# Kernel tuning notes

Measured on AMD Instinct MI355X. Metric: run time of the kernel, lower is better.

## Reference

```python
import jax, jax.numpy as jnp
import numpy as np
from jax import lax

# Static config (mirrors Caps2dMatwo init_kwargs)
K_SIZE = 5
T1 = 8              # num_capsule (output capsule types)
POS = (4, 4)
APP = (4, 4)
ROUTINGS = 3
COORD_ADD = True
ZP = POS[0] * POS[1]   # 16
ZA = APP[0] * APP[1]   # 16
Z = ZP + ZA            # 32 == input channels z_0


def _psquash(p, axis):
    return p / jnp.max(jnp.abs(p), axis=axis, keepdims=True)


def _matwo_squash(p, axis):
    n2 = jnp.sum(p * p, axis=axis, keepdims=True)
    n = jnp.sqrt(n2 + 1e-9)
    return n2 / (1.0 + n2) * p / n


def _coord_const(H, W):
    # coordinate_addition: adds normalized (x, y) into last row of the pos matrix
    yy, xx = np.meshgrid(np.arange(H), np.arange(W), indexing='ij')
    c = np.zeros((H * W, 1, POS[1], POS[1]), np.float32)
    c[:, 0, -1, 0] = xx.reshape(-1) / W
    c[:, 0, -1, 1] = yy.reshape(-1) / H
    return jnp.asarray(c)


def setup_inputs() -> dict:
    key = jax.random.key(0)
    k1, k2, k3, k4, k5 = jax.random.split(key, 5)
    N, T0, H, W = 4, 4, 96, 96
    return {
        'input_tensor': jax.random.normal(k1, (N, T0, Z, H, W), jnp.float32),
        'W_conv': jax.random.normal(k2, (T0, K_SIZE, K_SIZE, 1, T1), jnp.float32) * 0.05,
        'W_pos': jax.random.normal(k3, (T0, POS[1] * POS[1], T1), jnp.float32) * 0.05,
        'W_app': jax.random.normal(k4, (T0, APP[1] * APP[1], T1), jnp.float32) * 0.05,
        'b_app': jax.random.normal(k5, (T0, T1), jnp.float32) * 0.05,
    }


def reference(input_tensor, W_conv, W_pos, W_app, b_app):
    N, t0, z0, H, W = input_tensor.shape
    coord = _coord_const(H, W)
    u_hat_list = []
    for i in range(t0):
        # per input capsule type: spatial conv applied channel-wise
        u_t = input_tensor[:, i].reshape(N * z0, H, W, 1)
        u_spat = lax.conv_general_dilated(
            u_t, W_conv[i], (1, 1), 'SAME',
            dimension_numbers=('NHWC', 'HWIO', 'NHWC'))        # [N*z0, H, W, T1]
        u_spat = (u_spat.reshape(N, z0, H, W, T1)
                  .transpose(0, 2, 3, 4, 1)                    # [N,H,W,T1,z0]
                  .reshape(N, H, W, T1 * z0))
        u_pos = u_spat[..., :T1 * ZP].reshape(N, H, W, T1, POS[0], POS[1])
        u_app = u_spat[..., T1 * ZP:].reshape(N, H, W, T1, APP[0], APP[1])
        m_pos = W_pos[i].reshape(T1, POS[1], POS[1])
        m_app = W_app[i].reshape(T1, APP[1], APP[1])
        u_app = u_app + b_app[i].reshape(1, 1, 1, T1, 1, 1)
        # l2 normalize pos matrix along axis -2 (tf.l2_normalize semantics)
        m_pos = m_pos / jnp.sqrt(jnp.maximum(
            jnp.sum(m_pos * m_pos, axis=-2, keepdims=True), 1e-12))
        if COORD_ADD:
            m_pos = (m_pos + coord).reshape(1, H, W, T1, POS[1], POS[1])
        # matmult2d == batched matmul
        u_hat_pos = jnp.matmul(u_pos, m_pos).reshape(N, H, W, T1, ZP)
        u_hat_app = jnp.matmul(u_app, m_app).reshape(N, H, W, T1, ZA)
        u_hat_t = jnp.concatenate([u_hat_pos, u_hat_app], axis=-1)
        u_hat_list.append(u_hat_t.transpose(0, 4, 1, 2, 3))    # [N,Z,H,W,T1]
    u_hat = jnp.stack(u_hat_list, axis=-2)                     # [N,Z,H,W,t0,T1]

    # dual routing (sigmoid agreement), vectorized across output capsules
    u_pos_all = u_hat[:, :ZP]
    u_app_all = u_hat[:, ZP:]
    b = jnp.zeros((N, H, W, t0, T1), input_tensor.dtype)
    for _ in range(ROUTINGS - 1):
        r = jax.nn.sigmoid(b)                                  # [N,H,W,t0,T1]
        p = jnp.einsum('nzhwot,nhwot->tnzhw', u_hat, r)        # [T1,N,Z,H,W]
        v_pos = _psquash(p[:, :, :ZP], 2)
        v_app = _matwo_squash(p[:, :, ZP:], 2)
        rout = (jnp.einsum('nzhwot,tnzhw->nhwot', u_pos_all, v_pos)
                * jnp.einsum('nzhwot,tnzhw->nhwot', u_app_all, v_app))
        b = b + rout
    c = jax.nn.sigmoid(b)

    p = jnp.einsum('nzhwot,nhwot->tnzhw', u_hat, c)
    v_pos = _psquash(p[:, :, :ZP], 2)
    v_app = _matwo_squash(p[:, :, ZP:], 2)
    out = jnp.concatenate([v_pos, v_app], axis=2)              # [T1,N,Z,H,W]
    return out.transpose(1, 0, 2, 3, 4)                        # [N,T1,Z,H,W]
```

## Files before the change

### kernel.cpp

```cpp
#include <hip/hip_runtime.h>
#include <hip/hip_fp16.h>
#include <math.h>

#define IMG_H 96
#define IMG_W 96
#define HW (IMG_H * IMG_W)
#define TW 16
#define TH 2
#define TR (TH + 4)
#define TC 20
#define TS2 36

#define WS_MSH 400
#define WS_ASH 912

__device__ __forceinline__ float quad_sum(float v) {
    v += __int_as_float(__builtin_amdgcn_update_dpp(
            0, __float_as_int(v), 0xB1, 0xF, 0xF, true));
    v += __int_as_float(__builtin_amdgcn_update_dpp(
            0, __float_as_int(v), 0x4E, 0xF, 0xF, true));
    return v;
}
__device__ __forceinline__ float quad_max(float v) {
    v = fmaxf(v, __int_as_float(__builtin_amdgcn_update_dpp(
            0, __float_as_int(v), 0xB1, 0xF, 0xF, true)));
    v = fmaxf(v, __int_as_float(__builtin_amdgcn_update_dpp(
            0, __float_as_int(v), 0x4E, 0xF, 0xF, true)));
    return v;
}

__device__ __forceinline__ void route_store(const float (*uh)[8], int q, int nt,
                                            int pix, float* __restrict__ out)
{
    float bb[4] = {0.0f, 0.0f, 0.0f, 0.0f};
    #pragma unroll
    for (int it = 0; it < 2; ++it) {
        float r0 = 1.0f / (1.0f + __expf(-bb[0]));
        float r1 = 1.0f / (1.0f + __expf(-bb[1]));
        float r2 = 1.0f / (1.0f + __expf(-bb[2]));
        float r3 = 1.0f / (1.0f + __expf(-bb[3]));
        float pz[4], pa[4];
        #pragma unroll
        for (int j = 0; j < 4; ++j)
            pz[j] = fmaf(uh[0][j], r0, fmaf(uh[1][j], r1,
                    fmaf(uh[2][j], r2, uh[3][j] * r3)));
        float mx = quad_max(fmaxf(fmaxf(fabsf(pz[0]), fabsf(pz[1])),
                                  fmaxf(fabsf(pz[2]), fabsf(pz[3]))));
        float dp[4];
        #pragma unroll
        for (int o = 0; o < 4; ++o)
            dp[o] = quad_sum(fmaf(uh[o][0], pz[0], fmaf(uh[o][1], pz[1],
                             fmaf(uh[o][2], pz[2], uh[o][3] * pz[3]))));
        #pragma unroll
        for (int j = 0; j < 4; ++j)
            pa[j] = fmaf(uh[0][4 + j], r0, fmaf(uh[1][4 + j], r1,
                    fmaf(uh[2][4 + j], r2, uh[3][4 + j] * r3)));
        float n2 = quad_sum(fmaf(pa[0], pa[0], fmaf(pa[1], pa[1],
                            fmaf(pa[2], pa[2], pa[3] * pa[3]))));
        float invm = 1.0f / mx;
        float sc   = n2 / ((1.0f + n2) * sqrtf(n2 + 1e-9f));
        #pragma unroll
        for (int o = 0; o < 4; ++o) {
            float da = quad_sum(fmaf(uh[o][4], pa[0], fmaf(uh[o][5], pa[1],
                               fmaf(uh[o][6], pa[2], uh[o][7] * pa[3]))));
            bb[o] += (invm * dp[o]) * (sc * da);
        }
    }
    float r0 = 1.0f / (1.0f + __expf(-bb[0]));
    float r1 = 1.0f / (1.0f + __expf(-bb[1]));
    float r2 = 1.0f / (1.0f + __expf(-bb[2]));
    float r3 = 1.0f / (1.0f + __expf(-bb[3]));
    float pz[4], pa[4];
    #pragma unroll
    for (int j = 0; j < 4; ++j)
        pz[j] = fmaf(uh[0][j], r0, fmaf(uh[1][j], r1,
                fmaf(uh[2][j], r2, uh[3][j] * r3)));
    float mx = quad_max(fmaxf(fmaxf(fabsf(pz[0]), fabsf(pz[1])),
                              fmaxf(fabsf(pz[2]), fabsf(pz[3]))));
    #pragma unroll
    for (int j = 0; j < 4; ++j)
        pa[j] = fmaf(uh[0][4 + j], r0, fmaf(uh[1][4 + j], r1,
                fmaf(uh[2][4 + j], r2, uh[3][4 + j] * r3)));
    float n2 = quad_sum(fmaf(pa[0], pa[0], fmaf(pa[1], pa[1],
                        fmaf(pa[2], pa[2], pa[3] * pa[3]))));
    float invm = 1.0f / mx;
    float sc   = n2 / ((1.0f + n2) * sqrtf(n2 + 1e-9f));
    float* op = out + ((size_t)nt * 32 + (q << 2)) * HW + pix;
    op[0 * HW] = pz[0] * invm;
    op[1 * HW] = pz[1] * invm;
    op[2 * HW] = pz[2] * invm;
    op[3 * HW] = pz[3] * invm;
    op[16 * HW] = pa[0] * sc;
    op[17 * HW] = pa[1] * sc;
    op[18 * HW] = pa[2] * sc;
    op[19 * HW] = pa[3] * sc;
}

__global__ void __launch_bounds__(256)
caps_pack_kernel(const float* __restrict__ Wc, const float* __restrict__ Wp,
                 const float* __restrict__ Wa, float* __restrict__ ws)
{
    const int tid = threadIdx.x;
    for (int i = tid; i < 400; i += 256) {
        int fp  = i / 100;
        int rem = i - fp * 100;
        int tap = rem >> 2;
        int g   = i & 3;
        int oe  = (g & 1) << 1;
        int f   = fp + ((g >> 1) << 2);
        __half2 hv = __floats2half2_rn(Wc[oe * 200 + tap * 8 + f],
                                       Wc[(oe + 1) * 200 + tap * 8 + f]);
        ((__half2*)ws)[i] = hv;
    }
    if (tid < 128) {
        int c  = tid & 3;
        int tt = (tid >> 2) & 7;
        int oo = tid >> 5;
        const float* src = Wp + oo * 128 + tt * 16 + c;
        float v0 = src[0], v1 = src[4], v2 = src[8], v3 = src[12];
        float s = v0 * v0 + v1 * v1 + v2 * v2 + v3 * v3;
        float inv = 1.0f / sqrtf(fmaxf(s, 1e-12f));
        float* dst = ws + WS_MSH + (oo * 8 + tt) * 16 + c;
        dst[0] = v0 * inv; dst[4] = v1 * inv; dst[8] = v2 * inv; dst[12] = v3 * inv;
    } else {
        int i = tid - 128;
        ((float4*)(ws + WS_ASH))[i] = ((const float4*)Wa)[i];
    }
}

__global__ void __launch_bounds__(512)
caps_one_kernel(const float* __restrict__ x,
                const float* __restrict__ ws,
                const float* __restrict__ Ba,
                float* __restrict__ out)
{
    __shared__ __align__(16) __half2 tile2[TR * TC * TS2];

    const int tid    = threadIdx.x;
    const int q      = tid & 3;
    const int px     = (tid >> 2) & 15;
    const int wv     = tid >> 6;
    const int wb     = blockIdx.x * TW;
    const int h0     = blockIdx.y * TH;
    const int n      = blockIdx.z >> 1;
    const int parity = blockIdx.z & 1;
    const int t      = __builtin_amdgcn_readfirstlane(parity + 2 * (wv & 3));
    const int rr     = __builtin_amdgcn_readfirstlane(wv >> 2);
    const int w      = wb + px;
    const int h      = h0 + rr;

    {
        const int col = tid & 15;
        const int g   = tid >> 4;
        #pragma unroll
        for (int k = 0; k < 2; ++k) {
            int r = g + (k << 5);
            if (r < 48) {
                int dy    = r >> 3;
                int cpg   = r & 7;
                int hh    = h0 + dy - 2;
                int zq    = cpg >> 1;
                int cbase = (cpg & 1) << 1;
                int chan  = n * 128 + parity * 16 + zq * 4 + cbase;
                float v[8];
                #pragma unroll
                for (int j = 0; j < 8; ++j) v[j] = 0.0f;
                if ((unsigned)hh < IMG_H) {
                    const float* src = x + (size_t)chan * HW + hh * IMG_W + wb + col;
                    #pragma unroll
                    for (int j = 0; j < 8; ++j)
                        v[j] = src[(size_t)((j & 3) * 32 + (j >> 2)) * HW];
                }
                __half2 h4[4];
                #pragma unroll
                for (int j = 0; j < 4; ++j)
                    h4[j] = __floats2half2_rn(v[2 * j], v[2 * j + 1]);
                *(uint4*)&tile2[(dy * TC + 2 + col) * TS2 + (cpg << 2)] =
                    *(const uint4*)h4;
            }
        }
        const int m  = tid & 3;
        const int xx = (m < 2) ? m : (m + TW);
        const int ww = wb - 2 + xx;
        const int rh = tid >> 2;
        #pragma unroll
        for (int k = 0; k < 2; ++k) {
            int r = rh + (k << 7);
            if (r < 192) {
                int dy = r >> 5;
                int cp = r & 31;
                int hh = h0 + dy - 2;
                int o0 = (cp & 1) << 1;
                int c  = (cp >> 1) & 3;
                int zq = cp >> 3;
                int chan = n * 128 + o0 * 32 + parity * 16 + zq * 4 + c;
                float v0 = 0.0f, v1 = 0.0f;
                if ((unsigned)hh < IMG_H && (unsigned)ww < IMG_W) {
                    const float* src = x + (size_t)chan * HW + hh * IMG_W + ww;
                    v0 = src[0];
                    v1 = src[(size_t)32 * HW];
                }
                tile2[(dy * TC + xx) * TS2 + cp] = __floats2half2_rn(v0, v1);
            }
        }
    }
    __syncthreads();

    __half2 rp2[8], ra2[8];
    const __half2 z2 = __float2half2_rn(0.0f);
    #pragma unroll
    for (int i = 0; i < 8; ++i) { rp2[i] = z2; ra2[i] = z2; }

    const uint4* wq = (const uint4*)ws + (t >> 1) * 25;
    #pragma unroll 1
    for (int dy = 0; dy < 5; ++dy) {
        #pragma unroll
        for (int dx = 0; dx < 5; ++dx) {
            const __half2* t2 =
                &tile2[((rr + dy) * TC + px + dx) * TS2 + (q << 3)];
            union { uint4 u; __half2 hh[4]; } A, B, Wt;
            A.u  = *(const uint4*)t2;
            B.u  = *(const uint4*)(t2 + 4);
            Wt.u = wq[dy * 5 + dx];
            rp2[0] = __hfma2(A.hh[0], Wt.hh[0], rp2[0]);
            rp2[1] = __hfma2(A.hh[1], Wt.hh[1], rp2[1]);
            rp2[2] = __hfma2(A.hh[2], Wt.hh[0], rp2[2]);
            rp2[3] = __hfma2(A.hh[3], Wt.hh[1], rp2[3]);
            rp2[4] = __hfma2(B.hh[0], Wt.hh[0], rp2[4]);
            rp2[5] = __hfma2(B.hh[1], Wt.hh[1], rp2[5]);
            rp2[6] = __hfma2(B.hh[2], Wt.hh[0], rp2[6]);
            rp2[7] = __hfma2(B.hh[3], Wt.hh[1], rp2[7]);
            ra2[0] = __hfma2(A.hh[0], Wt.hh[2], ra2[0]);
            ra2[1] = __hfma2(A.hh[1], Wt.hh[3], ra2[1]);
            ra2[2] = __hfma2(A.hh[2], Wt.hh[2], ra2[2]);
            ra2[3] = __hfma2(A.hh[3], Wt.hh[3], ra2[3]);
            ra2[4] = __hfma2(B.hh[0], Wt.hh[2], ra2[4]);
            ra2[5] = __hfma2(B.hh[1], Wt.hh[3], ra2[5]);
            ra2[6] = __hfma2(B.hh[2], Wt.hh[2], ra2[6]);
            ra2[7] = __hfma2(B.hh[3], Wt.hh[3], ra2[7]);
        }
    }

    float uh[4][8];
    {
        const float cx = (float)w * (1.0f / 96.0f);
        const float cy = (float)h * (1.0f / 96.0f);
        #pragma unroll
        for (int o = 0; o < 4; ++o) {
            const float* mb = ws + WS_MSH + (o * 8 + t) * 16;
            float4 m0 = *(const float4*)(mb + 0);
            float4 m1 = *(const float4*)(mb + 4);
            float4 m2 = *(const float4*)(mb + 8);
            float4 m3 = *(const float4*)(mb + 12);
            m3.x += cx;
            m3.y += cy;
            const int pr = o >> 1;
            float r0, r1, r2, r3;
            if (o & 1) {
                r0 = __high2float(rp2[0 + pr]); r1 = __high2float(rp2[2 + pr]);
                r2 = __high2float(rp2[4 + pr]); r3 = __high2float(rp2[6 + pr]);
            } else {
                r0 = __low2float(rp2[0 + pr]);  r1 = __low2float(rp2[2 + pr]);
                r2 = __low2float(rp2[4 + pr]);  r3 = __low2float(rp2[6 + pr]);
            }
            uh[o][0] = r0 * m0.x + r1 * m1.x + r2 * m2.x + r3 * m3.x;
            uh[o][1] = r0 * m0.y + r1 * m1.y + r2 * m2.y + r3 * m3.y;
            uh[o][2] = r0 * m0.z + r1 * m1.z + r2 * m2.z + r3 * m3.z;
            uh[o][3] = r0 * m0.w + r1 * m1.w + r2 * m2.w + r3 * m3.w;
        }
        #pragma unroll
        for (int o = 0; o < 4; ++o) {
            const float* ab = ws + WS_ASH + (o * 8 + t) * 16;
            float4 a0 = *(const float4*)(ab + 0);
            float4 a1 = *(const float4*)(ab + 4);
            float4 a2 = *(const float4*)(ab + 8);
            float4 a3 = *(const float4*)(ab + 12);
            const float bias = Ba[o * 8 + t];
            const int pr = o >> 1;
            float r0, r1, r2, r3;
            if (o & 1) {
                r0 = __high2float(ra2[0 + pr]); r1 = __high2float(ra2[2 + pr]);
                r2 = __high2float(ra2[4 + pr]); r3 = __high2float(ra2[6 + pr]);
            } else {
                r0 = __low2float(ra2[0 + pr]);  r1 = __low2float(ra2[2 + pr]);
                r2 = __low2float(ra2[4 + pr]);  r3 = __low2float(ra2[6 + pr]);
            }
            r0 += bias; r1 += bias; r2 += bias; r3 += bias;
            uh[o][4] = r0 * a0.x + r1 * a1.x + r2 * a2.x + r3 * a3.x;
            uh[o][5] = r0 * a0.y + r1 * a1.y + r2 * a2.y + r3 * a3.y;
            uh[o][6] = r0 * a0.z + r1 * a1.z + r2 * a2.z + r3 * a3.z;
            uh[o][7] = r0 * a0.w + r1 * a1.w + r2 * a2.w + r3 * a3.w;
        }
    }

    route_store(uh, q, n * 8 + t, h * IMG_W + w, out);
}

extern "C" void kernel_launch(void* const* d_in, const int* in_sizes, int n_in,
                              void* d_out, int out_size, void* d_ws, size_t ws_size,
                              hipStream_t stream) {
    const float* x  = (const float*)d_in[0];
    const float* Wc = (const float*)d_in[1];
    const float* Wp = (const float*)d_in[2];
    const float* Wa = (const float*)d_in[3];
    const float* Ba = (const float*)d_in[4];
    float* outp = (float*)d_out;
    float* ws   = (float*)d_ws;

    caps_pack_kernel<<<dim3(1), 256, 0, stream>>>(Wc, Wp, Wa, ws);
    caps_one_kernel<<<dim3(IMG_W / TW, IMG_H / TH, 8), 512, 0, stream>>>(
        x, ws, Ba, outp);
}
```

Measured before the change: 125.3 us.

## Compute two output capsule types per wave to reuse shared tile reads

Halves the block to 256 threads and has each wave compute two output capsule types (ta, tb) for its row, so each LDS load of the input tile feeds twice as many half2 FMAs. The tile loading loops are rebalanced across the smaller block, and the LDS row stride is padded from 36 to 40 half2, presumably to change bank mapping. This raises register pressure with four accumulator arrays and two weight vectors, and duplicates the routing epilogue per thread.

```diff
diff --git a/kernel.cpp b/kernel.cpp
--- a/kernel.cpp
+++ b/kernel.cpp
@@ -9,7 +9,7 @@
 #define TH 2
 #define TR (TH + 4)
 #define TC 20
-#define TS2 36
+#define TS2 40
 
 #define WS_MSH 400
 #define WS_ASH 912
@@ -96,6 +96,62 @@
     op[19 * HW] = pa[3] * sc;
 }
 
+__device__ __forceinline__ void emit_route(
+    const __half2* rp2, const __half2* ra2,
+    const float* __restrict__ ws, const float* __restrict__ Ba,
+    int t, int q, int nt, int pix, float cx, float cy,
+    float* __restrict__ out)
+{
+    float uh[4][8];
+    #pragma unroll
+    for (int o = 0; o < 4; ++o) {
+        const float* mb = ws + WS_MSH + (o * 8 + t) * 16;
+        float4 m0 = *(const float4*)(mb + 0);
+        float4 m1 = *(const float4*)(mb + 4);
+        float4 m2 = *(const float4*)(mb + 8);
+        float4 m3 = *(const float4*)(mb + 12);
+        m3.x += cx;
+        m3.y += cy;
+        const int pr = o >> 1;
+        float r0, r1, r2, r3;
+        if (o & 1) {
+            r0 = __high2float(rp2[0 + pr]); r1 = __high2float(rp2[2 + pr]);
+            r2 = __high2float(rp2[4 + pr]); r3 = __high2float(rp2[6 + pr]);
+        } else {
+            r0 = __low2float(rp2[0 + pr]);  r1 = __low2float(rp2[2 + pr]);
+            r2 = __low2float(rp2[4 + pr]);  r3 = __low2float(rp2[6 + pr]);
+        }
+        uh[o][0] = r0 * m0.x + r1 * m1.x + r2 * m2.x + r3 * m3.x;
+        uh[o][1] = r0 * m0.y + r1 * m1.y + r2 * m2.y + r3 * m3.y;
+        uh[o][2] = r0 * m0.z + r1 * m1.z + r2 * m2.z + r3 * m3.z;
+        uh[o][3] = r0 * m0.w + r1 * m1.w + r2 * m2.w + r3 * m3.w;
+    }
+    #pragma unroll
+    for (int o = 0; o < 4; ++o) {
+        const float* ab = ws + WS_ASH + (o * 8 + t) * 16;
+        float4 a0 = *(const float4*)(ab + 0);
+        float4 a1 = *(const float4*)(ab + 4);
+        float4 a2 = *(const float4*)(ab + 8);
+        float4 a3 = *(const float4*)(ab + 12);
+        const float bias = Ba[o * 8 + t];
+        const int pr = o >> 1;
+        float r0, r1, r2, r3;
+        if (o & 1) {
+            r0 = __high2float(ra2[0 + pr]); r1 = __high2float(ra2[2 + pr]);
+            r2 = __high2float(ra2[4 + pr]); r3 = __high2float(ra2[6 + pr]);
+        } else {
+            r0 = __low2float(ra2[0 + pr]);  r1 = __low2float(ra2[2 + pr]);
+            r2 = __low2float(ra2[4 + pr]);  r3 = __low2float(ra2[6 + pr]);
+        }
+        r0 += bias; r1 += bias; r2 += bias; r3 += bias;
+        uh[o][4] = r0 * a0.x + r1 * a1.x + r2 * a2.x + r3 * a3.x;
+        uh[o][5] = r0 * a0.y + r1 * a1.y + r2 * a2.y + r3 * a3.y;
+        uh[o][6] = r0 * a0.z + r1 * a1.z + r2 * a2.z + r3 * a3.z;
+        uh[o][7] = r0 * a0.w + r1 * a1.w + r2 * a2.w + r3 * a3.w;
+    }
+    route_store(uh, q, nt, pix, out);
+}
+
 __global__ void __launch_bounds__(256)
 caps_pack_kernel(const float* __restrict__ Wc, const float* __restrict__ Wp,
                  const float* __restrict__ Wa, float* __restrict__ ws)
@@ -128,7 +184,7 @@
     }
 }
 
-__global__ void __launch_bounds__(512)
+__global__ void __launch_bounds__(256)
 caps_one_kernel(const float* __restrict__ x,
                 const float* __restrict__ ws,
                 const float* __restrict__ Ba,
@@ -144,8 +200,11 @@
     const int h0     = blockIdx.y * TH;
     const int n      = blockIdx.z >> 1;
     const int parity = blockIdx.z & 1;
-    const int t      = __builtin_amdgcn_readfirstlane(parity + 2 * (wv & 3));
-    const int rr     = __builtin_amdgcn_readfirstlane(wv >> 2);
+    const int rr     = __builtin_amdgcn_readfirstlane(wv >> 1);
+    const int sa     = __builtin_amdgcn_readfirstlane((wv & 1) << 1);
+    const int sb     = sa + 1;
+    const int ta     = parity + 2 * sa;
+    const int tb     = parity + 2 * sb;
     const int w      = wb + px;
     const int h      = h0 + rr;
 
@@ -153,147 +212,114 @@
         const int col = tid & 15;
         const int g   = tid >> 4;
         #pragma unroll
-        for (int k = 0; k < 2; ++k) {
-            int r = g + (k << 5);
-            if (r < 48) {
-                int dy    = r >> 3;
-                int cpg   = r & 7;
-                int hh    = h0 + dy - 2;
-                int zq    = cpg >> 1;
-                int cbase = (cpg & 1) << 1;
-                int chan  = n * 128 + parity * 16 + zq * 4 + cbase;
-                float v[8];
+        for (int k = 0; k < 3; ++k) {
+            int r = g + (k << 4);
+            int dy    = r >> 3;
+            int cpg   = r & 7;
+            int hh    = h0 + dy - 2;
+            int zq    = cpg >> 1;
+            int cbase = (cpg & 1) << 1;
+            int chan  = n * 128 + parity * 16 + zq * 4 + cbase;
+            float v[8];
+            #pragma unroll
+            for (int j = 0; j < 8; ++j) v[j] = 0.0f;
+            if ((unsigned)hh < IMG_H) {
+                const float* src = x + (size_t)chan * HW + hh * IMG_W + wb + col;
                 #pragma unroll
-                for (int j = 0; j < 8; ++j) v[j] = 0.0f;
-                if ((unsigned)hh < IMG_H) {
-                    const float* src = x + (size_t)chan * HW + hh * IMG_W + wb + col;
-                    #pragma unroll
-                    for (int j = 0; j < 8; ++j)
-                        v[j] = src[(size_t)((j & 3) * 32 + (j >> 2)) * HW];
-                }
-                __half2 h4[4];
-                #pragma unroll
-                for (int j = 0; j < 4; ++j)
-                    h4[j] = __floats2half2_rn(v[2 * j], v[2 * j + 1]);
-                *(uint4*)&tile2[(dy * TC + 2 + col) * TS2 + (cpg << 2)] =
-                    *(const uint4*)h4;
+                for (int j = 0; j < 8; ++j)
+                    v[j] = src[(size_t)((j & 3) * 32 + (j >> 2)) * HW];
             }
+            __half2 h4[4];
+            #pragma unroll
+            for (int j = 0; j < 4; ++j)
+                h4[j] = __floats2half2_rn(v[2 * j], v[2 * j + 1]);
+            *(uint4*)&tile2[(dy * TC + 2 + col) * TS2 + (cpg << 2)] =
+                *(const uint4*)h4;
         }
         const int m  = tid & 3;
         const int xx = (m < 2) ? m : (m + TW);
         const int ww = wb - 2 + xx;
         const int rh = tid >> 2;
         #pragma unroll
-        for (int k = 0; k < 2; ++k) {
-            int r = rh + (k << 7);
-            if (r < 192) {
-                int dy = r >> 5;
-                int cp = r & 31;
-                int hh = h0 + dy - 2;
-                int o0 = (cp & 1) << 1;
-                int c  = (cp >> 1) & 3;
-                int zq = cp >> 3;
-                int chan = n * 128 + o0 * 32 + parity * 16 + zq * 4 + c;
-                float v0 = 0.0f, v1 = 0.0f;
-                if ((unsigned)hh < IMG_H && (unsigned)ww < IMG_W) {
-                    const float* src = x + (size_t)chan * HW + hh * IMG_W + ww;
-                    v0 = src[0];
-                    v1 = src[(size_t)32 * HW];
-                }
-                tile2[(dy * TC + xx) * TS2 + cp] = __floats2half2_rn(v0, v1);
+        for (int k = 0; k < 3; ++k) {
+            int r = rh + (k << 6);
+            int dy = r >> 5;
+            int cp = r & 31;
+            int hh = h0 + dy - 2;
+            int o0 = (cp & 1) << 1;
+            int c  = (cp >> 1) & 3;
+            int zq = cp >> 3;
+            int chan = n * 128 + o0 * 32 + parity * 16 + zq * 4 + c;
+            float v0 = 0.0f, v1 = 0.0f;
+            if ((unsigned)hh < IMG_H && (unsigned)ww < IMG_W) {
+                const float* src = x + (size_t)chan * HW + hh * IMG_W + ww;
+                v0 = src[0];
+                v1 = src[(size_t)32 * HW];
             }
+            tile2[(dy * TC + xx) * TS2 + cp] = __floats2half2_rn(v0, v1);
         }
     }
     __syncthreads();
 
-    __half2 rp2[8], ra2[8];
+    __half2 rpa[8], raa[8], rpb[8], rab[8];
     const __half2 z2 = __float2half2_rn(0.0f);
     #pragma unroll
-    for (int i = 0; i < 8; ++i) { rp2[i] = z2; ra2[i] = z2; }
-
-    const uint4* wq = (const uint4*)ws + (t >> 1) * 25;
+    for (int i = 0; i < 8; ++i) { rpa[i] = z2; raa[i] = z2; rpb[i] = z2; rab[i] = z2; }
+
+    const uint4* wqa = (const uint4*)ws + sa * 25;
+    const uint4* wqb = (const uint4*)ws + sb * 25;
     #pragma unroll 1
     for (int dy = 0; dy < 5; ++dy) {
         #pragma unroll
         for (int dx = 0; dx < 5; ++dx) {
             const __half2* t2 =
                 &tile2[((rr + dy) * TC + px + dx) * TS2 + (q << 3)];
-            union { uint4 u; __half2 hh[4]; } A, B, Wt;
-            A.u  = *(const uint4*)t2;
-            B.u  = *(const uint4*)(t2 + 4);
-            Wt.u = wq[dy * 5 + dx];
-            rp2[0] = __hfma2(A.hh[0], Wt.hh[0], rp2[0]);
-            rp2[1] = __hfma2(A.hh[1], Wt.hh[1], rp2[1]);
-            rp2[2] = __hfma2(A.hh[2], Wt.hh[0], rp2[2]);
-            rp2[3] = __hfma2(A.hh[3], Wt.hh[1], rp2[3]);
-            rp2[4] = __hfma2(B.hh[0], Wt.hh[0], rp2[4]);
-            rp2[5] = __hfma2(B.hh[1], Wt.hh[1], rp2[5]);
-            rp2[6] = __hfma2(B.hh[2], Wt.hh[0], rp2[6]);
-            rp2[7] = __hfma2(B.hh[3], Wt.hh[1], rp2[7]);
-            ra2[0] = __hfma2(A.hh[0], Wt.hh[2], ra2[0]);
-            ra2[1] = __hfma2(A.hh[1], Wt.hh[3], ra2[1]);
-            ra2[2] = __hfma2(A.hh[2], Wt.hh[2], ra2[2]);
-            ra2[3] = __hfma2(A.hh[3], Wt.hh[3], ra2[3]);
-            ra2[4] = __hfma2(B.hh[0], Wt.hh[2], ra2[4]);
-            ra2[5] = __hfma2(B.hh[1], Wt.hh[3], ra2[5]);
-            ra2[6] = __hfma2(B.hh[2], Wt.hh[2], ra2[6]);
-            ra2[7] = __hfma2(B.hh[3], Wt.hh[3], ra2[7]);
-        }
-    }
-
-    float uh[4][8];
-    {
-        const float cx = (float)w * (1.0f / 96.0f);
-        const float cy = (float)h * (1.0f / 96.0f);
-        #pragma unroll
-        for (int o = 0; o < 4; ++o) {
-            const float* mb = ws + WS_MSH + (o * 8 + t) * 16;
-            float4 m0 = *(const float4*)(mb + 0);
-            float4 m1 = *(const float4*)(mb + 4);
-            float4 m2 = *(const float4*)(mb + 8);
-            float4 m3 = *(const float4*)(mb + 12);
-            m3.x += cx;
-            m3.y += cy;
-            const int pr = o >> 1;
-            float r0, r1, r2, r3;
-            if (o & 1) {
-                r0 = __high2float(rp2[0 + pr]); r1 = __high2float(rp2[2 + pr]);
-                r2 = __high2float(rp2[4 + pr]); r3 = __high2float(rp2[6 + pr]);
-            } else {
-                r0 = __low2float(rp2[0 + pr]);  r1 = __low2float(rp2[2 + pr]);
-                r2 = __low2float(rp2[4 + pr]);  r3 = __low2float(rp2[6 + pr]);
-            }
-            uh[o][0] = r0 * m0.x + r1 * m1.x + r2 * m2.x + r3 * m3.x;
-            uh[o][1] = r0 * m0.y + r1 * m1.y + r2 * m2.y + r3 * m3.y;
-            uh[o][2] = r0 * m0.z + r1 * m1.z + r2 * m2.z + r3 * m3.z;
-            uh[o][3] = r0 * m0.w + r1 * m1.w + r2 * m2.w + r3 * m3.w;
-        }
-        #pragma unroll
-        for (int o = 0; o < 4; ++o) {
-            const float* ab = ws + WS_ASH + (o * 8 + t) * 16;
-            float4 a0 = *(const float4*)(ab + 0);
-            float4 a1 = *(const float4*)(ab + 4);
-            float4 a2 = *(const float4*)(ab + 8);
-            float4 a3 = *(const float4*)(ab + 12);
-            const float bias = Ba[o * 8 + t];
-            const int pr = o >> 1;
-            float r0, r1, r2, r3;
-            if (o & 1) {
-                r0 = __high2float(ra2[0 + pr]); r1 = __high2float(ra2[2 + pr]);
-                r2 = __high2float(ra2[4 + pr]); r3 = __high2float(ra2[6 + pr]);
-            } else {
-                r0 = __low2float(ra2[0 + pr]);  r1 = __low2float(ra2[2 + pr]);
-                r2 = __low2float(ra2[4 + pr]);  r3 = __low2float(ra2[6 + pr]);
-            }
-            r0 += bias; r1 += bias; r2 += bias; r3 += bias;
-            uh[o][4] = r0 * a0.x + r1 * a1.x + r2 * a2.x + r3 * a3.x;
-            uh[o][5] = r0 * a0.y + r1 * a1.y + r2 * a2.y + r3 * a3.y;
-            uh[o][6] = r0 * a0.z + r1 * a1.z + r2 * a2.z + r3 * a3.z;
-            uh[o][7] = r0 * a0.w + r1 * a1.w + r2 * a2.w + r3 * a3.w;
-        }
-    }
-
-    route_store(uh, q, n * 8 + t, h * IMG_W + w, out);
+            union { uint4 u; __half2 hh[4]; } A, B, Wa_, Wb_;
+            A.u   = *(const uint4*)t2;
+            B.u   = *(const uint4*)(t2 + 4);
+            Wa_.u = wqa[dy * 5 + dx];
+            Wb_.u = wqb[dy * 5 + dx];
+            rpa[0] = __hfma2(A.hh[0], Wa_.hh[0], rpa[0]);
+            rpa[1] = __hfma2(A.hh[1], Wa_.hh[1], rpa[1]);
+            rpa[2] = __hfma2(A.hh[2], Wa_.hh[0], rpa[2]);
+            rpa[3] = __hfma2(A.hh[3], Wa_.hh[1], rpa[3]);
+            rpa[4] = __hfma2(B.hh[0], Wa_.hh[0], rpa[4]);
+            rpa[5] = __hfma2(B.hh[1], Wa_.hh[1], rpa[5]);
+            rpa[6] = __hfma2(B.hh[2], Wa_.hh[0], rpa[6]);
+            rpa[7] = __hfma2(B.hh[3], Wa_.hh[1], rpa[7]);
+            raa[0] = __hfma2(A.hh[0], Wa_.hh[2], raa[0]);
+            raa[1] = __hfma2(A.hh[1], Wa_.hh[3], raa[1]);
+            raa[2] = __hfma2(A.hh[2], Wa_.hh[2], raa[2]);
+            raa[3] = __hfma2(A.hh[3], Wa_.hh[3], raa[3]);
+            raa[4] = __hfma2(B.hh[0], Wa_.hh[2], raa[4]);
+            raa[5] = __hfma2(B.hh[1], Wa_.hh[3], raa[5]);
+            raa[6] = __hfma2(B.hh[2], Wa_.hh[2], raa[6]);
+            raa[7] = __hfma2(B.hh[3], Wa_.hh[3], raa[7]);
+            rpb[0] = __hfma2(A.hh[0], Wb_.hh[0], rpb[0]);
+            rpb[1] = __hfma2(A.hh[1], Wb_.hh[1], rpb[1]);
+            rpb[2] = __hfma2(A.hh[2], Wb_.hh[0], rpb[2]);
+            rpb[3] = __hfma2(A.hh[3], Wb_.hh[1], rpb[3]);
+            rpb[4] = __hfma2(B.hh[0], Wb_.hh[0], rpb[4]);
+            rpb[5] = __hfma2(B.hh[1], Wb_.hh[1], rpb[5]);
+            rpb[6] = __hfma2(B.hh[2], Wb_.hh[0], rpb[6]);
+            rpb[7] = __hfma2(B.hh[3], Wb_.hh[1], rpb[7]);
+            rab[0] = __hfma2(A.hh[0], Wb_.hh[2], rab[0]);
+            rab[1] = __hfma2(A.hh[1], Wb_.hh[3], rab[1]);
+            rab[2] = __hfma2(A.hh[2], Wb_.hh[2], rab[2]);
+            rab[3] = __hfma2(A.hh[3], Wb_.hh[3], rab[3]);
+            rab[4] = __hfma2(B.hh[0], Wb_.hh[2], rab[4]);
+            rab[5] = __hfma2(B.hh[1], Wb_.hh[3], rab[5]);
+            rab[6] = __hfma2(B.hh[2], Wb_.hh[2], rab[6]);
+            rab[7] = __hfma2(B.hh[3], Wb_.hh[3], rab[7]);
+        }
+    }
+
+    const float cx = (float)w * (1.0f / 96.0f);
+    const float cy = (float)h * (1.0f / 96.0f);
+    const int pix = h * IMG_W + w;
+
+    emit_route(rpa, raa, ws, Ba, ta, q, n * 8 + ta, pix, cx, cy, out);
+    emit_route(rpb, rab, ws, Ba, tb, q, n * 8 + tb, pix, cx, cy, out);
 }
 
 extern "C" void kernel_launch(void* const* d_in, const int* in_sizes, int n_in,
@@ -308,6 +334,6 @@
     float* ws   = (float*)d_ws;
 
     caps_pack_kernel<<<dim3(1), 256, 0, stream>>>(Wc, Wp, Wa, ws);
-    caps_one_kernel<<<dim3(IMG_W / TW, IMG_H / TH, 8), 512, 0, stream>>>(
+    caps_one_kernel<<<dim3(IMG_W / TW, IMG_H / TH, 8), 256, 0, stream>>>(
         x, ws, Ba, outp);
 }
```

New measurement: 133.1 us. 6.2% more time.

## Double tile height to 1024-thread blocks and register-prefetch conv rows

Applied to the files above, without the earlier changes.

Doubles the output rows per block (TH 2→4) and launches 1024-thread blocks. The tile loader loops collapse to one load per thread because the thread count now exactly covers the interior and halo rows. The 5x5 conv loop is fully unrolled, and each next tile row is prefetched from shared memory into registers (ping-pong buffers) while the current row is being computed. The aim is to spread the halo load over more output rows and to hide LDS latency. The risks are higher register pressure and possible spills, partly because of the aggressive __launch_bounds__(1024, 4) occupancy hint, and a halved grid size.

```diff
diff --git a/kernel.cpp b/kernel.cpp
--- a/kernel.cpp
+++ b/kernel.cpp
@@ -6,7 +6,7 @@
 #define IMG_W 96
 #define HW (IMG_H * IMG_W)
 #define TW 16
-#define TH 2
+#define TH 4
 #define TR (TH + 4)
 #define TC 20
 #define TS2 36
@@ -128,7 +128,7 @@
     }
 }
 
-__global__ void __launch_bounds__(512)
+__global__ void __launch_bounds__(1024, 4)
 caps_one_kernel(const float* __restrict__ x,
                 const float* __restrict__ ws,
                 const float* __restrict__ Ba,
@@ -152,57 +152,46 @@
     {
         const int col = tid & 15;
         const int g   = tid >> 4;
-        #pragma unroll
-        for (int k = 0; k < 2; ++k) {
-            int r = g + (k << 5);
-            if (r < 48) {
-                int dy    = r >> 3;
-                int cpg   = r & 7;
-                int hh    = h0 + dy - 2;
-                int zq    = cpg >> 1;
-                int cbase = (cpg & 1) << 1;
-                int chan  = n * 128 + parity * 16 + zq * 4 + cbase;
-                float v[8];
-                #pragma unroll
-                for (int j = 0; j < 8; ++j) v[j] = 0.0f;
-                if ((unsigned)hh < IMG_H) {
-                    const float* src = x + (size_t)chan * HW + hh * IMG_W + wb + col;
-                    #pragma unroll
-                    for (int j = 0; j < 8; ++j)
-                        v[j] = src[(size_t)((j & 3) * 32 + (j >> 2)) * HW];
-                }
-                __half2 h4[4];
-                #pragma unroll
-                for (int j = 0; j < 4; ++j)
-                    h4[j] = __floats2half2_rn(v[2 * j], v[2 * j + 1]);
-                *(uint4*)&tile2[(dy * TC + 2 + col) * TS2 + (cpg << 2)] =
-                    *(const uint4*)h4;
-            }
-        }
+        const int dy    = g >> 3;
+        const int cpg   = g & 7;
+        const int hh    = h0 + dy - 2;
+        const int zq    = cpg >> 1;
+        const int cbase = (cpg & 1) << 1;
+        const int chan  = n * 128 + parity * 16 + zq * 4 + cbase;
+        float v[8];
+        #pragma unroll
+        for (int j = 0; j < 8; ++j) v[j] = 0.0f;
+        if ((unsigned)hh < IMG_H) {
+            const float* src = x + (size_t)chan * HW + hh * IMG_W + wb + col;
+            #pragma unroll
+            for (int j = 0; j < 8; ++j)
+                v[j] = src[(size_t)((j & 3) * 32 + (j >> 2)) * HW];
+        }
+        __half2 h4[4];
+        #pragma unroll
+        for (int j = 0; j < 4; ++j)
+            h4[j] = __floats2half2_rn(v[2 * j], v[2 * j + 1]);
+        *(uint4*)&tile2[(dy * TC + 2 + col) * TS2 + (cpg << 2)] =
+            *(const uint4*)h4;
+
         const int m  = tid & 3;
         const int xx = (m < 2) ? m : (m + TW);
         const int ww = wb - 2 + xx;
         const int rh = tid >> 2;
-        #pragma unroll
-        for (int k = 0; k < 2; ++k) {
-            int r = rh + (k << 7);
-            if (r < 192) {
-                int dy = r >> 5;
-                int cp = r & 31;
-                int hh = h0 + dy - 2;
-                int o0 = (cp & 1) << 1;
-                int c  = (cp >> 1) & 3;
-                int zq = cp >> 3;
-                int chan = n * 128 + o0 * 32 + parity * 16 + zq * 4 + c;
-                float v0 = 0.0f, v1 = 0.0f;
-                if ((unsigned)hh < IMG_H && (unsigned)ww < IMG_W) {
-                    const float* src = x + (size_t)chan * HW + hh * IMG_W + ww;
-                    v0 = src[0];
-                    v1 = src[(size_t)32 * HW];
-                }
-                tile2[(dy * TC + xx) * TS2 + cp] = __floats2half2_rn(v0, v1);
-            }
-        }
+        const int hdy = rh >> 5;
+        const int cp  = rh & 31;
+        const int hhh = h0 + hdy - 2;
+        const int o0  = (cp & 1) << 1;
+        const int hc  = (cp >> 1) & 3;
+        const int hzq = cp >> 3;
+        const int hchan = n * 128 + o0 * 32 + parity * 16 + hzq * 4 + hc;
+        float v0 = 0.0f, v1 = 0.0f;
+        if ((unsigned)hhh < IMG_H && (unsigned)ww < IMG_W) {
+            const float* src = x + (size_t)hchan * HW + hhh * IMG_W + ww;
+            v0 = src[0];
+            v1 = src[(size_t)32 * HW];
+        }
+        tile2[(hdy * TC + xx) * TS2 + cp] = __floats2half2_rn(v0, v1);
     }
     __syncthreads();
 
@@ -212,15 +201,33 @@
     for (int i = 0; i < 8; ++i) { rp2[i] = z2; ra2[i] = z2; }
 
     const uint4* wq = (const uint4*)ws + (t >> 1) * 25;
-    #pragma unroll 1
+
+    uint4 a0[5], b0[5], a1[5], b1[5];
+    #pragma unroll
+    for (int dx = 0; dx < 5; ++dx) {
+        const __half2* t2 = &tile2[(rr * TC + px + dx) * TS2 + (q << 3)];
+        a0[dx] = *(const uint4*)t2;
+        b0[dx] = *(const uint4*)(t2 + 4);
+    }
+    #pragma unroll
     for (int dy = 0; dy < 5; ++dy) {
+        if (dy < 4) {
+            #pragma unroll
+            for (int dx = 0; dx < 5; ++dx) {
+                const __half2* t2 =
+                    &tile2[((rr + dy + 1) * TC + px + dx) * TS2 + (q << 3)];
+                if ((dy & 1) == 0) {
+                    a1[dx] = *(const uint4*)t2; b1[dx] = *(const uint4*)(t2 + 4);
+                } else {
+                    a0[dx] = *(const uint4*)t2; b0[dx] = *(const uint4*)(t2 + 4);
+                }
+            }
+        }
         #pragma unroll
         for (int dx = 0; dx < 5; ++dx) {
-            const __half2* t2 =
-                &tile2[((rr + dy) * TC + px + dx) * TS2 + (q << 3)];
             union { uint4 u; __half2 hh[4]; } A, B, Wt;
-            A.u  = *(const uint4*)t2;
-            B.u  = *(const uint4*)(t2 + 4);
+            A.u  = (dy & 1) ? a1[dx] : a0[dx];
+            B.u  = (dy & 1) ? b1[dx] : b0[dx];
             Wt.u = wq[dy * 5 + dx];
             rp2[0] = __hfma2(A.hh[0], Wt.hh[0], rp2[0]);
             rp2[1] = __hfma2(A.hh[1], Wt.hh[1], rp2[1]);
@@ -271,10 +278,10 @@
         #pragma unroll
         for (int o = 0; o < 4; ++o) {
             const float* ab = ws + WS_ASH + (o * 8 + t) * 16;
-            float4 a0 = *(const float4*)(ab + 0);
-            float4 a1 = *(const float4*)(ab + 4);
-            float4 a2 = *(const float4*)(ab + 8);
-            float4 a3 = *(const float4*)(ab + 12);
+            float4 a0_ = *(const float4*)(ab + 0);
+            float4 a1_ = *(const float4*)(ab + 4);
+            float4 a2_ = *(const float4*)(ab + 8);
+            float4 a3_ = *(const float4*)(ab + 12);
             const float bias = Ba[o * 8 + t];
             const int pr = o >> 1;
             float r0, r1, r2, r3;
@@ -286,10 +293,10 @@
                 r2 = __low2float(ra2[4 + pr]);  r3 = __low2float(ra2[6 + pr]);
             }
             r0 += bias; r1 += bias; r2 += bias; r3 += bias;
-            uh[o][4] = r0 * a0.x + r1 * a1.x + r2 * a2.x + r3 * a3.x;
-            uh[o][5] = r0 * a0.y + r1 * a1.y + r2 * a2.y + r3 * a3.y;
-            uh[o][6] = r0 * a0.z + r1 * a1.z + r2 * a2.z + r3 * a3.z;
-            uh[o][7] = r0 * a0.w + r1 * a1.w + r2 * a2.w + r3 * a3.w;
+            uh[o][4] = r0 * a0_.x + r1 * a1_.x + r2 * a2_.x + r3 * a3_.x;
+            uh[o][5] = r0 * a0_.y + r1 * a1_.y + r2 * a2_.y + r3 * a3_.y;
+            uh[o][6] = r0 * a0_.z + r1 * a1_.z + r2 * a2_.z + r3 * a3_.z;
+            uh[o][7] = r0 * a0_.w + r1 * a1_.w + r2 * a2_.w + r3 * a3_.w;
         }
     }
 
@@ -308,6 +315,6 @@
     float* ws   = (float*)d_ws;
 
     caps_pack_kernel<<<dim3(1), 256, 0, stream>>>(Wc, Wp, Wa, ws);
-    caps_one_kernel<<<dim3(IMG_W / TW, IMG_H / TH, 8), 512, 0, stream>>>(
+    caps_one_kernel<<<dim3(IMG_W / TW, IMG_H / TH, 8), 1024, 0, stream>>>(
         x, ws, Ba, outp);
 }
```

Measured after the change: 128.9 us. +2.8%, slower.
